# Kernel optimization log

Hardware: AMD Instinct MI355X
Metric: run time of the kernel (lower is better)

Reference implementation:

```python
import jax, jax.numpy as jnp
import numpy as np

HW, B, C, NH, NC, HF, WF = 2500, 2, 256, 8, 6, 64, 176
DFF = 4 * C
EPS = 1e-5

def _layernorm(x, g, b):
    m = x.mean(-1, keepdims=True)
    v = ((x - m) ** 2).mean(-1, keepdims=True)
    return (x - m) / jnp.sqrt(v + EPS) * g + b

def _mha(q, kv, in_w, in_b, ow, ob):
    # q: [L,B,C], kv: [S,B,C] (batch_first=False, torch nn.MultiheadAttention)
    L, Bq, Cq = q.shape
    S = kv.shape[0]
    Dh = Cq // NH
    qp = (q @ in_w[:Cq].T + in_b[:Cq]).reshape(L, Bq, NH, Dh)
    kp = (kv @ in_w[Cq:2 * Cq].T + in_b[Cq:2 * Cq]).reshape(S, Bq, NH, Dh)
    vp = (kv @ in_w[2 * Cq:].T + in_b[2 * Cq:]).reshape(S, Bq, NH, Dh)
    att = jnp.einsum('lbhd,sbhd->bhls', qp, kp) * (1.0 / np.sqrt(Dh))
    att = jax.nn.softmax(att, axis=-1)
    out = jnp.einsum('bhls,sbhd->lbhd', att, vp).reshape(L, Bq, Cq)
    return out @ ow.T + ob

def _grid_sample_zeros(feat, grid):
    # feat: [B,N,C,H,W], grid: [B,N,Q,2] in [-1,1]; bilinear, align_corners=False, zero padding
    Bb, N, Cc, Hf, Wf = feat.shape
    Q = grid.shape[2]
    x = (grid[..., 0] + 1.0) * (Wf / 2.0) - 0.5
    y = (grid[..., 1] + 1.0) * (Hf / 2.0) - 0.5
    x0 = jnp.floor(x); y0 = jnp.floor(y)
    wx = x - x0; wy = y - y0
    x0i = x0.astype(jnp.int32); y0i = y0.astype(jnp.int32)
    ff = feat.reshape(Bb, N, Cc, Hf * Wf)
    def corner(xi, yi, w):
        valid = (xi >= 0) & (xi < Wf) & (yi >= 0) & (yi < Hf)
        idx = jnp.clip(yi, 0, Hf - 1) * Wf + jnp.clip(xi, 0, Wf - 1)  # [B,N,Q]
        g = jnp.take_along_axis(ff, jnp.broadcast_to(idx[:, :, None, :], (Bb, N, Cc, Q)), axis=-1)
        return g * (w * valid)[:, :, None, :]
    return (corner(x0i, y0i, (1.0 - wx) * (1.0 - wy)) + corner(x0i + 1, y0i, wx * (1.0 - wy))
            + corner(x0i, y0i + 1, (1.0 - wx) * wy) + corner(x0i + 1, y0i + 1, wx * wy))

def _forward(bev_queries, prev_bev, image_feat, reference_points, camera_intrinsics, camera_extrinsics,
             in_proj_w, in_proj_b, out_proj_w, out_proj_b, tsa_norm_g, tsa_norm_b,
             sca_w, sca_b, sca_norm_g, sca_norm_b, ffn_w1, ffn_b1, ffn_w2, ffn_b2, ffn_norm_g, ffn_norm_b):
    # TSA (dropout is identity in eval)
    tsa_out = _mha(bev_queries, prev_bev, in_proj_w, in_proj_b, out_proj_w, out_proj_b)
    x = _layernorm(bev_queries + tsa_out, tsa_norm_g, tsa_norm_b)
    # SCA: ego->camera->image projection
    R = camera_extrinsics[:, :, :3, :3]            # [B,N,3,3]
    t = camera_extrinsics[:, :, :3, 3]             # [B,N,3]
    R_e2c = jnp.swapaxes(R, -1, -2)
    t_e2c = -jnp.einsum('bnij,bnj->bni', R_e2c, t)
    pts_cam = jnp.einsum('bnij,qj->bnqi', R_e2c, reference_points) + t_e2c[:, :, None, :]  # [B,N,Q,3]
    pts_img = jnp.einsum('bnij,bnqj->bnqi', camera_intrinsics, pts_cam)
    uv = pts_img[..., :2] / jnp.maximum(pts_img[..., 2:3], 1e-5)
    grid = jnp.stack([2.0 * uv[..., 0] / WF - 1.0, 2.0 * uv[..., 1] / HF - 1.0], axis=-1)  # [B,N,Q,2]
    Bq = bev_queries.shape[1]
    feat_r = image_feat.reshape(Bq, NC, C, HF, WF)
    sampled = _grid_sample_zeros(feat_r, grid).mean(axis=1)   # [B,C,Q]
    sampled = jnp.transpose(sampled, (2, 0, 1))               # [Q,B,C]
    sca_out = sampled @ sca_w.T + sca_b
    x = _layernorm(x + sca_out, sca_norm_g, sca_norm_b)
    # FFN (torch nn.GELU default = exact erf)
    h = jax.nn.gelu(x @ ffn_w1 + ffn_b1, approximate=False)
    ffn_out = h @ ffn_w2 + ffn_b2
    return _layernorm(x + ffn_out, ffn_norm_g, ffn_norm_b)

def setup_inputs():
    key = jax.random.key(0)
    ks = jax.random.split(key, 16)
    f = jnp.float32
    s = 0.02
    return {
        'bev_queries': jax.random.normal(ks[0], (HW, B, C), f),
        'prev_bev': jax.random.normal(ks[1], (HW, B, C), f),
        'image_feat': jax.random.normal(ks[2], (B * NC, C, HF, WF), f),
        'reference_points': jax.random.normal(ks[3], (HW, 3), f) * 20.0,
        'camera_intrinsics': jax.random.normal(ks[4], (B, NC, 3, 3), f),
        'camera_extrinsics': jax.random.normal(ks[5], (B, NC, 4, 4), f),
        'spatial_shapes': jnp.array([[HF, WF]], jnp.int32),
        'in_proj_w': jax.random.normal(ks[6], (3 * C, C), f) * s,
        'in_proj_b': jnp.zeros((3 * C,), f),
        'out_proj_w': jax.random.normal(ks[7], (C, C), f) * s,
        'out_proj_b': jnp.zeros((C,), f),
        'tsa_norm_g': jnp.ones((C,), f), 'tsa_norm_b': jnp.zeros((C,), f),
        'sca_w': jax.random.normal(ks[8], (C, C), f) * s,
        'sca_b': jnp.zeros((C,), f),
        'sca_norm_g': jnp.ones((C,), f), 'sca_norm_b': jnp.zeros((C,), f),
        'ffn_w1': jax.random.normal(ks[9], (C, DFF), f) * s,
        'ffn_b1': jnp.zeros((DFF,), f),
        'ffn_w2': jax.random.normal(ks[10], (DFF, C), f) * s,
        'ffn_b2': jnp.zeros((C,), f),
        'ffn_norm_g': jnp.ones((C,), f), 'ffn_norm_b': jnp.zeros((C,), f),
    }

def reference(bev_queries, prev_bev, image_feat, reference_points, camera_intrinsics, camera_extrinsics,
              in_proj_w, in_proj_b, out_proj_w, out_proj_b, tsa_norm_g, tsa_norm_b,
              sca_w, sca_b, sca_norm_g, sca_norm_b, ffn_w1, ffn_b1, ffn_w2, ffn_b2, ffn_norm_g, ffn_norm_b,
              spatial_shapes):
    return _forward(bev_queries, prev_bev, image_feat, reference_points, camera_intrinsics, camera_extrinsics,
                    in_proj_w, in_proj_b, out_proj_w, out_proj_b, tsa_norm_g, tsa_norm_b,
                    sca_w, sca_b, sca_norm_g, sca_norm_b, ffn_w1, ffn_b1, ffn_w2, ffn_b2, ffn_norm_g, ffn_norm_b)
```

## Files before the change

kernel.cpp:

```cpp
#include <hip/hip_runtime.h>

typedef unsigned short u16;
typedef __attribute__((ext_vector_type(8))) __bf16 bf8_t;
typedef __attribute__((ext_vector_type(4))) float f4_t;

union bf8u { u16 u[8]; bf8_t v; uint4 q; };

__device__ __forceinline__ float bf2f(u16 v) {
  return __uint_as_float(((unsigned int)v) << 16);
}
__device__ __forceinline__ u16 f2bf(float f) {
  unsigned int u = __float_as_uint(f);
  unsigned int r = u + 0x7FFFu + ((u >> 16) & 1u);
  return (u16)(r >> 16);
}
__device__ __forceinline__ float bflo(unsigned int w) { return __uint_as_float(w << 16); }
__device__ __forceinline__ float bfhi(unsigned int w) { return __uint_as_float(w & 0xFFFF0000u); }
__device__ __forceinline__ float ldf1(const void* p, size_t i, int isf32) {
  return isf32 ? ((const float*)p)[i] : bf2f(((const u16*)p)[i]);
}

#define LQ    2500
#define LQP   2560
#define BB    2
#define CC    256
#define NCC   6
#define HFF   64
#define WFF   176
#define DFF   1024
#define MROWS 5000

#define WB_UV   256
#define WB_WQKV 240256
#define WB_WOP  633472
#define WB_WSC  764544
#define WB_WF1  895616
#define WB_WF2  1419904
#define WB_S1   1944192
#define WB_S2   (WB_S1 + 2621440)
#define WB_S3   (WB_S2 + 2621440)
#define WB_VT   (WB_S3 + 2621440)
#define WB_H    WB_S2
#define WB_Y3   (WB_S2 + 10485760)

__global__ void detect_k(const u16* __restrict__ rp, int* __restrict__ flag) {
  int bad = 0;
  for (int i = threadIdx.x; i < 7500; i += 64) {
    float v = bf2f(rp[i]);
    if (!(fabsf(v) < 1e6f)) bad = 1;
  }
  int anybad = __any(bad);
  if (threadIdx.x == 0) flag[0] = anybad ? 1 : 0;
}

struct WDesc {
  const void* src[6];
  u16* dst[6];
  int n[6];
  int mode[6];
  int Kd[6], Nd[6];
};
__global__ __launch_bounds__(256) void cvtw_k(WDesc d, const int* __restrict__ flag) {
  const int df = flag[0];
  const int i = blockIdx.y;
  const int n = d.n[i];
  for (int j = blockIdx.x * 256 + threadIdx.x; j < n; j += gridDim.x * 256) {
    if (d.mode[i] == 2) {
      const int row = j / (LQP - LQ), col = LQ + j % (LQP - LQ);
      d.dst[i][(size_t)row * LQP + col] = 0;
    } else if (d.mode[i] == 1) {
      const int K = d.Kd[i], N = d.Nd[i];
      const int nn = j / K, kk = j - nn * K;
      d.dst[i][j] = f2bf(ldf1(d.src[i], (size_t)kk * N + nn, df));
    } else {
      d.dst[i][j] = f2bf(ldf1(d.src[i], j, df));
    }
  }
}

template<int KTPL, int XRAW, int ACT, int RES, int STORE_T>
__global__ __launch_bounds__(64) void gemm_nl(
    const void* __restrict__ Xv, const u16* __restrict__ W,
    const void* __restrict__ bias, size_t boff,
    const void* __restrict__ resv,
    u16* __restrict__ Y, int M, int N, const int* __restrict__ flag)
{
  const int df = flag[0];
  const int lane = threadIdx.x;
  const int ln15 = lane & 15, l4 = lane >> 4;
  const int m0 = blockIdx.x * 16, n0 = blockIdx.y * 64;
  const int am = min(m0 + ln15, M - 1);

  f4_t acc[4];
#pragma unroll
  for (int nt = 0; nt < 4; ++nt) acc[nt] = (f4_t){0.f, 0.f, 0.f, 0.f};

#pragma unroll 8
  for (int k0 = 0; k0 < KTPL; k0 += 32) {
    bf8u a;
    if (XRAW && df) {
      const float* p = (const float*)Xv + (size_t)am * KTPL + k0 + l4 * 8;
      float4 r0 = *(const float4*)p, r1 = *(const float4*)(p + 4);
      a.u[0]=f2bf(r0.x); a.u[1]=f2bf(r0.y); a.u[2]=f2bf(r0.z); a.u[3]=f2bf(r0.w);
      a.u[4]=f2bf(r1.x); a.u[5]=f2bf(r1.y); a.u[6]=f2bf(r1.z); a.u[7]=f2bf(r1.w);
    } else {
      a.q = *(const uint4*)((const u16*)Xv + (size_t)am * KTPL + k0 + l4 * 8);
    }
#pragma unroll
    for (int nt = 0; nt < 4; ++nt) {
      bf8u b;
      b.q = *(const uint4*)&W[(size_t)(n0 + nt * 16 + ln15) * KTPL + k0 + l4 * 8];
      acc[nt] = __builtin_amdgcn_mfma_f32_16x16x32_bf16(a.v, b.v, acc[nt], 0, 0, 0);
    }
  }
#pragma unroll
  for (int nt = 0; nt < 4; ++nt) {
    const int gn = n0 + nt * 16 + ln15;
    const float bv = ldf1(bias, boff + gn, df);
#pragma unroll
    for (int r = 0; r < 4; ++r) {
      const int gm = m0 + l4 * 4 + r;
      if (gm < M) {
        float x = acc[nt][r] + bv;
        if (ACT) x = 0.5f * x * (1.f + erff(x * 0.70710678118654752f));
        if (RES == 1)      x += bf2f(((const u16*)resv)[(size_t)gm * N + gn]);
        else if (RES == 2) x += ldf1(resv, (size_t)gm * N + gn, df);
        if (STORE_T) Y[(size_t)(gn + (gm & 1) * 256) * LQP + (gm >> 1)] = f2bf(x);
        else         Y[(size_t)gm * N + gn] = f2bf(x);
      }
    }
  }
}

#define TPW 10
__global__ __launch_bounds__(256) void attn_mf(
    const u16* __restrict__ Qw, const u16* __restrict__ Kw,
    const u16* __restrict__ Vt, u16* __restrict__ Ow)
{
  __shared__ __align__(16) u16 sP[4][16 * 72];
  __shared__ float sO[4][16][32];
  __shared__ float sM[4][16];
  __shared__ float sL[4][16];
  const int t = threadIdx.x;
  const int lane = t & 63, w = t >> 6;
  const int ln15 = lane & 15, l4 = lane >> 4;
  const int q0 = blockIdx.x * 16;
  const int by = blockIdx.y;
  const int b = by >> 3, h = by & 7;
  u16* myP = &sP[w][0];
  const float SCL2E = 0.25505654481f;

  bf8u aq;
  {
    const int qrow = min(q0 + ln15, LQ - 1);
    bf8u qr; qr.q = *(const uint4*)&Qw[((size_t)qrow * BB + b) * CC + h * 32 + l4 * 8];
#pragma unroll
    for (int i = 0; i < 8; ++i) aq.u[i] = f2bf(bf2f(qr.u[i]) * SCL2E);
  }

  f4_t oacc[2];
  oacc[0] = (f4_t){0.f,0.f,0.f,0.f};
  oacc[1] = (f4_t){0.f,0.f,0.f,0.f};
  float m_r[4] = {-1e30f, -1e30f, -1e30f, -1e30f};
  float l_r[4] = {0.f, 0.f, 0.f, 0.f};

  for (int kt = w * TPW; kt < w * TPW + TPW; ++kt) {
    const int kb = kt * 64;
    f4_t sv[4];
#pragma unroll
    for (int nt = 0; nt < 4; ++nt) {
      bf8u bk;
      bk.q = *(const uint4*)&Kw[((size_t)(kb + nt * 16 + ln15) * BB + b) * CC + h * 32 + l4 * 8];
      f4_t z = (f4_t){0.f,0.f,0.f,0.f};
      sv[nt] = __builtin_amdgcn_mfma_f32_16x16x32_bf16(aq.v, bk.v, z, 0, 0, 0);
    }
    float p[4][4];
    if (kb + 64 <= LQ) {
#pragma unroll
      for (int nt = 0; nt < 4; ++nt)
#pragma unroll
        for (int r = 0; r < 4; ++r) p[nt][r] = sv[nt][r];
    } else {
#pragma unroll
      for (int nt = 0; nt < 4; ++nt) {
        const bool ok = (kb + nt * 16 + ln15) < LQ;
#pragma unroll
        for (int r = 0; r < 4; ++r) p[nt][r] = ok ? sv[nt][r] : -1e30f;
      }
    }
#pragma unroll
    for (int r = 0; r < 4; ++r) {
      float mloc = fmaxf(fmaxf(p[0][r], p[1][r]), fmaxf(p[2][r], p[3][r]));
      mloc = fmaxf(mloc, __shfl_xor(mloc, 1));
      mloc = fmaxf(mloc, __shfl_xor(mloc, 2));
      mloc = fmaxf(mloc, __shfl_xor(mloc, 4));
      mloc = fmaxf(mloc, __shfl_xor(mloc, 8));
      const float mn = fmaxf(m_r[r], mloc);
      const float alpha = __builtin_amdgcn_exp2f(m_r[r] - mn);
      m_r[r] = mn;
      float s = 0.f;
#pragma unroll
      for (int nt = 0; nt < 4; ++nt) {
        const float e = __builtin_amdgcn_exp2f(p[nt][r] - mn);
        p[nt][r] = e; s += e;
      }
      s += __shfl_xor(s, 1);
      s += __shfl_xor(s, 2);
      s += __shfl_xor(s, 4);
      s += __shfl_xor(s, 8);
      l_r[r] = l_r[r] * alpha + s;
      oacc[0][r] *= alpha;
      oacc[1][r] *= alpha;
    }
#pragma unroll
    for (int nt = 0; nt < 4; ++nt)
#pragma unroll
      for (int r = 0; r < 4; ++r)
        myP[(l4 * 4 + r) * 72 + nt * 16 + ln15] = f2bf(p[nt][r]);
#pragma unroll
    for (int ks = 0; ks < 2; ++ks) {
      bf8u ap;
      ap.q = *(const uint4*)&myP[ln15 * 72 + ks * 32 + l4 * 8];
#pragma unroll
      for (int nt = 0; nt < 2; ++nt) {
        bf8u bv;
        bv.q = *(const uint4*)&Vt[(size_t)(by * 32 + nt * 16 + ln15) * LQP + kb + ks * 32 + l4 * 8];
        oacc[nt] = __builtin_amdgcn_mfma_f32_16x16x32_bf16(ap.v, bv.v, oacc[nt], 0, 0, 0);
      }
    }
  }
#pragma unroll
  for (int nt = 0; nt < 2; ++nt)
#pragma unroll
    for (int r = 0; r < 4; ++r)
      sO[w][l4 * 4 + r][nt * 16 + ln15] = oacc[nt][r];
  if (ln15 == 0) {
#pragma unroll
    for (int r = 0; r < 4; ++r) { sM[w][l4 * 4 + r] = m_r[r]; sL[w][l4 * 4 + r] = l_r[r]; }
  }
  __syncthreads();
#pragma unroll
  for (int i = t; i < 512; i += 256) {
    const int row = i >> 5, col = i & 31;
    const float M = fmaxf(fmaxf(sM[0][row], sM[1][row]), fmaxf(sM[2][row], sM[3][row]));
    float l = 0.f, O = 0.f;
#pragma unroll
    for (int w4 = 0; w4 < 4; ++w4) {
      const float sc = __builtin_amdgcn_exp2f(sM[w4][row] - M);
      l += sc * sL[w4][row];
      O += sc * sO[w4][row][col];
    }
    const int q = q0 + row;
    if (q < LQ)
      Ow[((size_t)q * BB + b) * CC + h * 32 + col] = f2bf(O / l);
  }
}

template<int TOOUT>
__global__ __launch_bounds__(256) void ln_k(const u16* __restrict__ X,
    const void* __restrict__ g, const void* __restrict__ be,
    void* __restrict__ Yv, int rows, const int* __restrict__ flag)
{
  const int df = flag[0];
  const int lane = threadIdx.x & 63;
  const int row = blockIdx.x * 4 + (threadIdx.x >> 6);
  if (row >= rows) return;
  uint2 raw = *(const uint2*)(X + (size_t)row * CC + lane * 4);
  float vx = bflo(raw.x), vy = bfhi(raw.x), vz = bflo(raw.y), vw = bfhi(raw.y);
  float s = vx + vy + vz + vw;
#pragma unroll
  for (int o = 1; o < 64; o <<= 1) s += __shfl_xor(s, o);
  const float mean = s * 0.00390625f;
  const float dx = vx - mean, dy = vy - mean, dz = vz - mean, dw = vw - mean;
  float sq = dx*dx + dy*dy + dz*dz + dw*dw;
#pragma unroll
  for (int o = 1; o < 64; o <<= 1) sq += __shfl_xor(sq, o);
  const float rstd = rsqrtf(sq * 0.00390625f + 1e-5f);
  const float g0 = ldf1(g, lane*4+0, df), g1 = ldf1(g, lane*4+1, df);
  const float g2 = ldf1(g, lane*4+2, df), g3 = ldf1(g, lane*4+3, df);
  const float b0 = ldf1(be, lane*4+0, df), b1 = ldf1(be, lane*4+1, df);
  const float b2 = ldf1(be, lane*4+2, df), b3 = ldf1(be, lane*4+3, df);
  const float y0 = dx * rstd * g0 + b0;
  const float y1 = dy * rstd * g1 + b1;
  const float y2 = dz * rstd * g2 + b2;
  const float y3 = dw * rstd * g3 + b3;
  if (TOOUT && df) {
    float* yp = (float*)Yv + (size_t)row * CC + lane * 4;
    *(float4*)yp = make_float4(y0, y1, y2, y3);
  } else {
    u16* yp = (u16*)Yv + (size_t)row * CC + lane * 4;
    unsigned int lo = (unsigned int)f2bf(y0) | ((unsigned int)f2bf(y1) << 16);
    unsigned int hi = (unsigned int)f2bf(y2) | ((unsigned int)f2bf(y3) << 16);
    *(uint2*)yp = make_uint2(lo, hi);
  }
}

__global__ __launch_bounds__(256) void uv_k(
    const void* __restrict__ refp, const void* __restrict__ intr,
    const void* __restrict__ extr, float* __restrict__ uv,
    const int* __restrict__ flag)
{
  const int df = flag[0];
  const int idx = blockIdx.x * 256 + threadIdx.x;
  if (idx >= BB * NCC * LQ) return;
  const int bc = idx / LQ;
  const int q = idx - bc * LQ;
  float R[3][3], tv[3], Kc[3][3], p[3];
#pragma unroll
  for (int i = 0; i < 3; ++i) {
#pragma unroll
    for (int j = 0; j < 3; ++j) {
      R[i][j] = ldf1(extr, bc*16 + i*4 + j, df);
      Kc[i][j] = ldf1(intr, bc*9 + i*3 + j, df);
    }
    tv[i] = ldf1(extr, bc*16 + i*4 + 3, df);
  }
#pragma unroll
  for (int j = 0; j < 3; ++j) p[j] = ldf1(refp, q*3 + j, df) - tv[j];
  float pc[3];
#pragma unroll
  for (int i = 0; i < 3; ++i) pc[i] = R[0][i]*p[0] + R[1][i]*p[1] + R[2][i]*p[2];
  float im[3];
#pragma unroll
  for (int i = 0; i < 3; ++i) im[i] = Kc[i][0]*pc[0] + Kc[i][1]*pc[1] + Kc[i][2]*pc[2];
  const float z = fmaxf(im[2], 1e-5f);
  uv[(size_t)idx*2 + 0] = im[0] / z - 0.5f;
  uv[(size_t)idx*2 + 1] = im[1] / z - 0.5f;
}

__global__ __launch_bounds__(256) void samp_k(
    const void* __restrict__ feat, const float* __restrict__ uv,
    u16* __restrict__ S, const int* __restrict__ flag)
{
  const int df = flag[0];
  const int c = blockIdx.x;
  const int b = blockIdx.y / 5;
  const int ch = blockIdx.y % 5;
  const int qend = min((ch + 1) * 500, LQ);
  for (int q = ch * 500 + threadIdx.x; q < qend; q += 256) {
    float acc = 0.f;
#pragma unroll
    for (int cam = 0; cam < NCC; ++cam) {
      const int bc = b * NCC + cam;
      const float x = uv[((size_t)bc * LQ + q) * 2 + 0];
      const float y = uv[((size_t)bc * LQ + q) * 2 + 1];
      const float xf = floorf(x), yf = floorf(y);
      const int x0 = (int)xf, y0 = (int)yf;
      const float wx = x - xf, wy = y - yf;
      const size_t base = ((size_t)bc * CC + c) * (HFF * WFF);
      const bool vx0 = (x0 >= 0) & (x0 < WFF);
      const bool vx1 = (x0 + 1 >= 0) & (x0 + 1 < WFF);
      const bool vy0 = (y0 >= 0) & (y0 < HFF);
      const bool vy1 = (y0 + 1 >= 0) & (y0 + 1 < HFF);
      if (vy0) {
        const size_t rb = base + (size_t)y0 * WFF;
        if (vx0) acc += (1.f - wx) * (1.f - wy) * ldf1(feat, rb + x0, df);
        if (vx1) acc += wx * (1.f - wy) * ldf1(feat, rb + x0 + 1, df);
      }
      if (vy1) {
        const size_t rb = base + (size_t)(y0 + 1) * WFF;
        if (vx0) acc += (1.f - wx) * wy * ldf1(feat, rb + x0, df);
        if (vx1) acc += wx * wy * ldf1(feat, rb + x0 + 1, df);
      }
    }
    S[((size_t)q * BB + b) * CC + c] = f2bf(acc * (1.f / 6.f));
  }
}

extern "C" void kernel_launch(void* const* d_in, const int* in_sizes, int n_in,
                              void* d_out, int out_size, void* d_ws, size_t ws_size,
                              hipStream_t stream) {
  (void)in_sizes; (void)n_in; (void)out_size; (void)ws_size;
  char* base = (char*)d_ws;
  int* flag = (int*)base;
  float* UV = (float*)(base + WB_UV);
  u16* WQKV = (u16*)(base + WB_WQKV);
  u16* WOP  = (u16*)(base + WB_WOP);
  u16* WSC  = (u16*)(base + WB_WSC);
  u16* WF1  = (u16*)(base + WB_WF1);
  u16* WF2  = (u16*)(base + WB_WF2);
  u16* S1 = (u16*)(base + WB_S1);
  u16* S2 = (u16*)(base + WB_S2);
  u16* S3 = (u16*)(base + WB_S3);
  u16* VT = (u16*)(base + WB_VT);
  u16* H  = (u16*)(base + WB_H);
  u16* Y3 = (u16*)(base + WB_Y3);

  detect_k<<<1, 64, 0, stream>>>((const u16*)d_in[3], flag);

  WDesc wd;
  wd.src[0] = d_in[7];  wd.dst[0] = WQKV; wd.n[0] = 196608; wd.mode[0] = 0; wd.Kd[0] = 0;    wd.Nd[0] = 0;
  wd.src[1] = d_in[9];  wd.dst[1] = WOP;  wd.n[1] = 65536;  wd.mode[1] = 0; wd.Kd[1] = 0;    wd.Nd[1] = 0;
  wd.src[2] = d_in[13]; wd.dst[2] = WSC;  wd.n[2] = 65536;  wd.mode[2] = 0; wd.Kd[2] = 0;    wd.Nd[2] = 0;
  wd.src[3] = d_in[17]; wd.dst[3] = WF1;  wd.n[3] = 262144; wd.mode[3] = 1; wd.Kd[3] = 256;  wd.Nd[3] = 1024;
  wd.src[4] = d_in[19]; wd.dst[4] = WF2;  wd.n[4] = 262144; wd.mode[4] = 1; wd.Kd[4] = 1024; wd.Nd[4] = 256;
  wd.src[5] = nullptr;  wd.dst[5] = VT;   wd.n[5] = 512 * (LQP - LQ); wd.mode[5] = 2; wd.Kd[5] = 0; wd.Nd[5] = 0;
  cvtw_k<<<dim3(128, 6), 256, 0, stream>>>(wd, flag);

  uv_k<<<(BB * NCC * LQ + 255) / 256, 256, 0, stream>>>(d_in[3], d_in[4], d_in[5], UV, flag);

  gemm_nl<256,1,0,0,0><<<dim3(313, 4), 64, 0, stream>>>(d_in[0], WQKV,          d_in[8], 0,   nullptr, S1, MROWS, CC, flag);
  gemm_nl<256,1,0,0,0><<<dim3(313, 4), 64, 0, stream>>>(d_in[1], WQKV + 65536,  d_in[8], 256, nullptr, S2, MROWS, CC, flag);
  gemm_nl<256,1,0,0,1><<<dim3(313, 4), 64, 0, stream>>>(d_in[1], WQKV + 131072, d_in[8], 512, nullptr, VT, MROWS, CC, flag);

  attn_mf<<<dim3(157, 16), 256, 0, stream>>>(S1, S2, VT, S3);

  gemm_nl<256,0,0,2,0><<<dim3(313, 4), 64, 0, stream>>>(S3, WOP, d_in[10], 0, d_in[0], S1, MROWS, CC, flag);
  ln_k<0><<<1250, 256, 0, stream>>>(S1, d_in[11], d_in[12], S2, MROWS, flag);

  samp_k<<<dim3(CC, BB * 5), 256, 0, stream>>>(d_in[2], UV, VT, flag);

  gemm_nl<256,0,0,1,0><<<dim3(313, 4), 64, 0, stream>>>(VT, WSC, d_in[14], 0, S2, S3, MROWS, CC, flag);
  ln_k<0><<<1250, 256, 0, stream>>>(S3, d_in[15], d_in[16], S1, MROWS, flag);

  gemm_nl<256,0,1,0,0><<<dim3(313, 16), 64, 0, stream>>>(S1, WF1, d_in[18], 0, nullptr, H,  MROWS, DFF, flag);
  gemm_nl<1024,0,0,1,0><<<dim3(313, 4),  64, 0, stream>>>(H,  WF2, d_in[20], 0, S1,      Y3, MROWS, CC,  flag);
  ln_k<1><<<1250, 256, 0, stream>>>(Y3, d_in[21], d_in[22], d_out, MROWS, flag);
}
```

Baseline: 523.1 us.

## Transpose attention MFMA operands so softmax stats stay per-lane, use hardware bf16 convert

Swaps the A/B operands of the QK^T and PV MFMAs so each lane holds one query row across its four accumulator registers. The row max and sum then reduce with only two cross-lane shuffles instead of four per register, and one running max/sum scalar replaces four. The P tile is written to LDS as packed 8-byte stores with a padded stride of 80, and the output staging buffer is padded to 33 columns to cut bank conflicts. The manual round-to-nearest-even bf16 conversion is replaced with a native __bf16 cast, which may use a hardware convert instruction.

```diff
diff --git a/kernel.cpp b/kernel.cpp
--- a/kernel.cpp
+++ b/kernel.cpp
@@ -10,9 +10,9 @@
   return __uint_as_float(((unsigned int)v) << 16);
 }
 __device__ __forceinline__ u16 f2bf(float f) {
-  unsigned int u = __float_as_uint(f);
-  unsigned int r = u + 0x7FFFu + ((u >> 16) & 1u);
-  return (u16)(r >> 16);
+  union { __bf16 h; u16 u; } c;
+  c.h = (__bf16)f;
+  return c.u;
 }
 __device__ __forceinline__ float bflo(unsigned int w) { return __uint_as_float(w << 16); }
 __device__ __forceinline__ float bfhi(unsigned int w) { return __uint_as_float(w & 0xFFFF0000u); }
@@ -137,8 +137,8 @@
     const u16* __restrict__ Qw, const u16* __restrict__ Kw,
     const u16* __restrict__ Vt, u16* __restrict__ Ow)
 {
-  __shared__ __align__(16) u16 sP[4][16 * 72];
-  __shared__ float sO[4][16][32];
+  __shared__ __align__(16) u16 sP[4][16 * 80];
+  __shared__ float sO[4][16][33];
   __shared__ float sM[4][16];
   __shared__ float sL[4][16];
   const int t = threadIdx.x;
@@ -161,8 +161,8 @@
   f4_t oacc[2];
   oacc[0] = (f4_t){0.f,0.f,0.f,0.f};
   oacc[1] = (f4_t){0.f,0.f,0.f,0.f};
-  float m_r[4] = {-1e30f, -1e30f, -1e30f, -1e30f};
-  float l_r[4] = {0.f, 0.f, 0.f, 0.f};
+  float m_r = -1e30f;
+  float l_r = 0.f;
 
   for (int kt = w * TPW; kt < w * TPW + TPW; ++kt) {
     const int kb = kt * 64;
@@ -172,7 +172,7 @@
       bf8u bk;
       bk.q = *(const uint4*)&Kw[((size_t)(kb + nt * 16 + ln15) * BB + b) * CC + h * 32 + l4 * 8];
       f4_t z = (f4_t){0.f,0.f,0.f,0.f};
-      sv[nt] = __builtin_amdgcn_mfma_f32_16x16x32_bf16(aq.v, bk.v, z, 0, 0, 0);
+      sv[nt] = __builtin_amdgcn_mfma_f32_16x16x32_bf16(bk.v, aq.v, z, 0, 0, 0);
     }
     float p[4][4];
     if (kb + 64 <= LQ) {
@@ -182,62 +182,62 @@
         for (int r = 0; r < 4; ++r) p[nt][r] = sv[nt][r];
     } else {
 #pragma unroll
-      for (int nt = 0; nt < 4; ++nt) {
-        const bool ok = (kb + nt * 16 + ln15) < LQ;
-#pragma unroll
-        for (int r = 0; r < 4; ++r) p[nt][r] = ok ? sv[nt][r] : -1e30f;
+      for (int nt = 0; nt < 4; ++nt)
+#pragma unroll
+        for (int r = 0; r < 4; ++r)
+          p[nt][r] = (kb + nt * 16 + l4 * 4 + r < LQ) ? sv[nt][r] : -1e30f;
+    }
+    const float m0 = fmaxf(fmaxf(p[0][0], p[0][1]), fmaxf(p[0][2], p[0][3]));
+    const float m1 = fmaxf(fmaxf(p[1][0], p[1][1]), fmaxf(p[1][2], p[1][3]));
+    const float m2 = fmaxf(fmaxf(p[2][0], p[2][1]), fmaxf(p[2][2], p[2][3]));
+    const float m3 = fmaxf(fmaxf(p[3][0], p[3][1]), fmaxf(p[3][2], p[3][3]));
+    float mloc = fmaxf(fmaxf(m0, m1), fmaxf(m2, m3));
+    mloc = fmaxf(mloc, __shfl_xor(mloc, 16));
+    mloc = fmaxf(mloc, __shfl_xor(mloc, 32));
+    const float mn = fmaxf(m_r, mloc);
+    const float alpha = __builtin_amdgcn_exp2f(m_r - mn);
+    m_r = mn;
+    float s = 0.f;
+#pragma unroll
+    for (int nt = 0; nt < 4; ++nt) {
+      float sn = 0.f;
+#pragma unroll
+      for (int r = 0; r < 4; ++r) {
+        const float e = __builtin_amdgcn_exp2f(p[nt][r] - mn);
+        p[nt][r] = e; sn += e;
       }
-    }
-#pragma unroll
-    for (int r = 0; r < 4; ++r) {
-      float mloc = fmaxf(fmaxf(p[0][r], p[1][r]), fmaxf(p[2][r], p[3][r]));
-      mloc = fmaxf(mloc, __shfl_xor(mloc, 1));
-      mloc = fmaxf(mloc, __shfl_xor(mloc, 2));
-      mloc = fmaxf(mloc, __shfl_xor(mloc, 4));
-      mloc = fmaxf(mloc, __shfl_xor(mloc, 8));
-      const float mn = fmaxf(m_r[r], mloc);
-      const float alpha = __builtin_amdgcn_exp2f(m_r[r] - mn);
-      m_r[r] = mn;
-      float s = 0.f;
-#pragma unroll
-      for (int nt = 0; nt < 4; ++nt) {
-        const float e = __builtin_amdgcn_exp2f(p[nt][r] - mn);
-        p[nt][r] = e; s += e;
+      s += sn;
+    }
+    s += __shfl_xor(s, 16);
+    s += __shfl_xor(s, 32);
+    l_r = l_r * alpha + s;
+#pragma unroll
+    for (int r = 0; r < 4; ++r) { oacc[0][r] *= alpha; oacc[1][r] *= alpha; }
+#pragma unroll
+    for (int nt = 0; nt < 4; ++nt) {
+      union { u16 h[4]; uint2 w2; } pk;
+#pragma unroll
+      for (int r = 0; r < 4; ++r) pk.h[r] = f2bf(p[nt][r]);
+      *(uint2*)&myP[ln15 * 80 + nt * 16 + l4 * 4] = pk.w2;
+    }
+#pragma unroll
+    for (int m = 0; m < 2; ++m) {
+      bf8u bp;
+      bp.q = *(const uint4*)&myP[ln15 * 80 + m * 32 + l4 * 8];
+#pragma unroll
+      for (int dt = 0; dt < 2; ++dt) {
+        bf8u av;
+        av.q = *(const uint4*)&Vt[(size_t)(by * 32 + dt * 16 + ln15) * LQP + kb + m * 32 + l4 * 8];
+        oacc[dt] = __builtin_amdgcn_mfma_f32_16x16x32_bf16(av.v, bp.v, oacc[dt], 0, 0, 0);
       }
-      s += __shfl_xor(s, 1);
-      s += __shfl_xor(s, 2);
-      s += __shfl_xor(s, 4);
-      s += __shfl_xor(s, 8);
-      l_r[r] = l_r[r] * alpha + s;
-      oacc[0][r] *= alpha;
-      oacc[1][r] *= alpha;
-    }
-#pragma unroll
-    for (int nt = 0; nt < 4; ++nt)
-#pragma unroll
-      for (int r = 0; r < 4; ++r)
-        myP[(l4 * 4 + r) * 72 + nt * 16 + ln15] = f2bf(p[nt][r]);
-#pragma unroll
-    for (int ks = 0; ks < 2; ++ks) {
-      bf8u ap;
-      ap.q = *(const uint4*)&myP[ln15 * 72 + ks * 32 + l4 * 8];
-#pragma unroll
-      for (int nt = 0; nt < 2; ++nt) {
-        bf8u bv;
-        bv.q = *(const uint4*)&Vt[(size_t)(by * 32 + nt * 16 + ln15) * LQP + kb + ks * 32 + l4 * 8];
-        oacc[nt] = __builtin_amdgcn_mfma_f32_16x16x32_bf16(ap.v, bv.v, oacc[nt], 0, 0, 0);
-      }
-    }
-  }
-#pragma unroll
-  for (int nt = 0; nt < 2; ++nt)
+    }
+  }
+#pragma unroll
+  for (int dt = 0; dt < 2; ++dt)
 #pragma unroll
     for (int r = 0; r < 4; ++r)
-      sO[w][l4 * 4 + r][nt * 16 + ln15] = oacc[nt][r];
-  if (ln15 == 0) {
-#pragma unroll
-    for (int r = 0; r < 4; ++r) { sM[w][l4 * 4 + r] = m_r[r]; sL[w][l4 * 4 + r] = l_r[r]; }
-  }
+      sO[w][ln15][dt * 16 + l4 * 4 + r] = oacc[dt][r];
+  if (l4 == 0) { sM[w][ln15] = m_r; sL[w][ln15] = l_r; }
   __syncthreads();
 #pragma unroll
   for (int i = t; i < 512; i += 256) {
```

New measurement: 520.4 us. No clear change (-0.5%).
